# Kernel tuning notes

Measured on AMD Instinct MI355X. Metric: run time of the kernel, lower is better.

Reference implementation:

```python
import jax, jax.numpy as jnp
import numpy as np

KH = KW = 3
K = KH * KW
GROUPS = 8


def conv_same(x, w, b=None):
    out = jax.lax.conv_general_dilated(x, w, (1, 1), 'SAME',
                                       dimension_numbers=('NHWC', 'HWIO', 'NHWC'))
    if b is not None:
        out = out + b
    return out


def feature_selection(x, w_att, w_sel):
    pooled = x.mean(axis=(1, 2), keepdims=True)            # [B,1,1,C]
    attn = jax.nn.sigmoid(conv_same(pooled, w_att))        # 1x1 conv, sigmoid
    return conv_same(x * (attn + 1.0), w_sel)              # [B,H,W,F]


def deform_sample(x, sy, sx):
    # x: [H,W,G,Cg]; sy,sx: [H,W,G,K] fractional sample coords (zero outside)
    H, W, G, _ = x.shape
    y0 = jnp.floor(sy)
    x0 = jnp.floor(sx)
    wy1 = sy - y0
    wx1 = sx - x0
    gi = jnp.arange(G)[None, None, :, None]

    def gather(yi, xi):
        valid = (yi >= 0) & (yi <= H - 1) & (xi >= 0) & (xi <= W - 1)
        yc = jnp.clip(yi, 0, H - 1).astype(jnp.int32)
        xc = jnp.clip(xi, 0, W - 1).astype(jnp.int32)
        v = x[yc, xc, gi]                                   # [H,W,G,K,Cg]
        return v * valid[..., None]

    v00 = gather(y0, x0)
    v01 = gather(y0, x0 + 1)
    v10 = gather(y0 + 1, x0)
    v11 = gather(y0 + 1, x0 + 1)
    wy1 = wy1[..., None]
    wx1 = wx1[..., None]
    top = v00 * (1 - wx1) + v01 * wx1
    bot = v10 * (1 - wx1) + v11 * wx1
    return top * (1 - wy1) + bot * wy1                      # [H,W,G,K,Cg]


def dcnv2(x, align, w_om, b_om, w_dcn, b_dcn):
    # x: [B,H,W,C] input to deform-conv; align: [B,H,W,Ca] alignment feature
    B, H, W, C = x.shape
    G = GROUPS
    Cg = C // G
    om = conv_same(align, w_om, b_om)                       # [B,H,W,G*3*K]
    off = om[..., :G * 2 * K].reshape(B, H, W, G, K, 2)     # (dy, dx)
    mask = jax.nn.sigmoid(om[..., G * 2 * K:]).reshape(B, H, W, G, K)

    iy = jnp.arange(H, dtype=x.dtype)[:, None, None, None]
    ix = jnp.arange(W, dtype=x.dtype)[None, :, None, None]
    ky, kx = jnp.meshgrid(jnp.arange(KH) - (KH - 1) // 2,
                          jnp.arange(KW) - (KW - 1) // 2, indexing='ij')
    ky = ky.reshape(K).astype(x.dtype)
    kx = kx.reshape(K).astype(x.dtype)
    sy = iy + ky + off[..., 0]                              # [B,H,W,G,K]
    sx = ix + kx + off[..., 1]

    xg = x.reshape(B, H, W, G, Cg)
    sampled = jax.vmap(deform_sample)(xg, sy, sx)           # [B,H,W,G,K,Cg]
    sampled = sampled * mask[..., None]
    sampled = sampled.transpose(0, 1, 2, 4, 3, 5).reshape(B, H, W, K, C)
    wk = w_dcn.reshape(K, C, -1)                            # [K,C,F]
    return jnp.einsum('bhwkc,kcf->bhwf', sampled, wk) + b_dcn


def reference(coarse, fine, w_att, w_sel, w_off, w_om, b_om, w_dcn, b_dcn):
    B, H, W, _ = fine.shape
    coarse_up = jax.image.resize(coarse, (B, H, W, coarse.shape[-1]), 'bilinear')
    fine_cal = feature_selection(fine, w_att, w_sel)
    fc = jnp.concatenate([fine_cal, coarse_up * 2.0], axis=-1)
    align = conv_same(fc, w_off)                            # 1x1, no bias
    aligned = jax.nn.relu(dcnv2(coarse_up, align, w_om, b_om, w_dcn, b_dcn))
    return aligned + fine_cal


def setup_inputs() -> dict:
    key = jax.random.key(0)
    ks = jax.random.split(key, 8)
    B, H, W = 4, 64, 64
    Cc, Cf, F = 256, 256, 256
    s = lambda fan: (2.0 / fan) ** 0.5
    return {
        'coarse': jax.random.normal(ks[0], (B, H // 2, W // 2, Cc), jnp.float32),
        'fine': jax.random.normal(ks[1], (B, H, W, Cf), jnp.float32),
        'w_att': jax.random.normal(ks[2], (1, 1, Cf, Cf), jnp.float32) * s(Cf),
        'w_sel': jax.random.normal(ks[3], (1, 1, Cf, F), jnp.float32) * s(Cf),
        'w_off': jax.random.normal(ks[4], (1, 1, F + Cc, 2 * F), jnp.float32) * s(F + Cc),
        'w_om': jax.random.normal(ks[5], (3, 3, 2 * F, GROUPS * 3 * K), jnp.float32) * 0.01,
        'b_om': jnp.zeros((GROUPS * 3 * K,), jnp.float32),
        'w_dcn': jax.random.normal(ks[6], (3, 3, Cc, F), jnp.float32) * s(9 * Cc),
        'b_dcn': jnp.zeros((F,), jnp.float32),
    }
```

## Files before the change

kernel.cpp:

```cpp
#include <hip/hip_runtime.h>
#include <hip/hip_bf16.h>
#include <cstddef>

constexpr int HWP = 64 * 64;
constexpr int CCH = 256;
constexpr int OMC = 216;
constexpr int KDC = 2304;

typedef __attribute__((ext_vector_type(8))) short bf16x8;
typedef __attribute__((ext_vector_type(4))) float f32x4;

__device__ inline unsigned short f2bf(float x) {
  __hip_bfloat16 h = __float2bfloat16(x);
  return *reinterpret_cast<unsigned short*>(&h);
}
__device__ inline float bf2f(unsigned short u) {
  unsigned int v = ((unsigned int)u) << 16;
  return __uint_as_float(v);
}
__device__ inline void bfpair(unsigned int u, float& a, float& b) {
  a = __uint_as_float(u << 16);
  b = __uint_as_float(u & 0xffff0000u);
}

__global__ __launch_bounds__(256) void prep_weights(
    const float* __restrict__ w_off, const float* __restrict__ w_om,
    const float* __restrict__ w_sel, const float* __restrict__ w_dcn,
    unsigned short* __restrict__ w_offT, unsigned short* __restrict__ w_omT,
    unsigned short* __restrict__ w_selT, unsigned short* __restrict__ w_dcnT) {
  int i = blockIdx.x * 256 + threadIdx.x;
  if (i < 512 * 512) {
    int n = i >> 9, k = i & 511;
    w_offT[i] = f2bf(w_off[k * 512 + n]);
  }
  if (i < 9 * 256 * 512) {
    int c = i & 511;
    int r = i >> 9;
    int tap = r >> 8;
    int n = r & 255;
    w_omT[i] = f2bf(n < OMC ? w_om[((size_t)tap * 512 + c) * OMC + n] : 0.f);
  }
  if (i < 256 * 256) {
    int n = i >> 8, k = i & 255;
    w_selT[i] = f2bf(w_sel[k * 256 + n]);
  }
  if (i < 9 * 256 * 256) {
    int tap = i >> 16, f = (i >> 8) & 255, c = i & 255;
    w_dcnT[i] = f2bf(w_dcn[((size_t)tap * 256 + c) * 256 + f]);
  }
}

__global__ __launch_bounds__(256) void pool_partial(
    const float* __restrict__ fine, float* __restrict__ partial) {
  int r = blockIdx.x;
  int b = blockIdx.y;
  int t = threadIdx.x;
  const float* src = fine + ((size_t)b * 4096 + r * 64) * 256 + t;
  float s = 0.f;
#pragma unroll 8
  for (int p = 0; p < 64; ++p) s += src[(size_t)p * 256];
  partial[((size_t)b * 64 + r) * 256 + t] = s;
}

__global__ __launch_bounds__(256) void pool_finish(
    const float* __restrict__ partial, const float* __restrict__ w_att,
    float* __restrict__ scale) {
  __shared__ float pl[256];
  int b = blockIdx.x;
  int t = threadIdx.x;
  const float* pp = partial + (size_t)b * 64 * 256 + t;
  float s = 0.f;
#pragma unroll 8
  for (int r = 0; r < 64; ++r) s += pp[(size_t)r * 256];
  pl[t] = s * (1.0f / 4096.0f);
  __syncthreads();
  float acc = 0.f;
  for (int ci = 0; ci < 256; ++ci) acc += pl[ci] * w_att[ci * 256 + t];
  scale[b * 256 + t] = 1.0f + 1.0f / (1.0f + expf(-acc));
}

__global__ __launch_bounds__(256) void upsample_kernel(
    const float* __restrict__ coarse, unsigned short* __restrict__ upbf,
    unsigned short* __restrict__ alignA) {
  int m = blockIdx.x;
  int c = threadIdx.x;
  int b = m >> 12, h = (m >> 6) & 63, w = m & 63;
  float cy = fminf(fmaxf(h * 0.5f - 0.25f, 0.f), 31.f);
  float cx = fminf(fmaxf(w * 0.5f - 0.25f, 0.f), 31.f);
  int y0 = (int)cy, x0 = (int)cx;
  float fy = cy - y0, fx = cx - x0;
  int y1 = min(y0 + 1, 31), x1 = min(x0 + 1, 31);
  const float* base = coarse + (size_t)b * 32 * 32 * CCH;
  float v00 = base[(y0 * 32 + x0) * CCH + c];
  float v01 = base[(y0 * 32 + x1) * CCH + c];
  float v10 = base[(y1 * 32 + x0) * CCH + c];
  float v11 = base[(y1 * 32 + x1) * CCH + c];
  float top = v00 + (v01 - v00) * fx;
  float bot = v10 + (v11 - v10) * fx;
  float v = top + (bot - top) * fy;
  upbf[(size_t)m * CCH + c] = f2bf(v);
  alignA[(size_t)m * 512 + 256 + c] = f2bf(2.f * v);
}

__global__ __launch_bounds__(256) void gemm_finecal_mfma(
    const float* __restrict__ fine, const float* __restrict__ scale,
    const unsigned short* __restrict__ w_selT,
    float* __restrict__ finecal, unsigned short* __restrict__ alignA) {
  __shared__ unsigned short As[128][72];
  __shared__ unsigned short Bs[64][72];
  __shared__ float sc[256];
  int n0 = blockIdx.x * 64;
  int m0 = blockIdx.y * 128;
  int t = threadIdx.x;
  int wid = t >> 6, lane = t & 63;
  int lrow = lane & 15, lq = lane >> 4;
  int bb = m0 >> 12;
  sc[t] = scale[bb * 256 + t];
  f32x4 acc[2][4];
#pragma unroll
  for (int i = 0; i < 2; ++i)
#pragma unroll
    for (int j = 0; j < 4; ++j) acc[i][j] = (f32x4){0.f, 0.f, 0.f, 0.f};
  for (int k0 = 0; k0 < 256; k0 += 64) {
    __syncthreads();
    for (int u = t; u < 128 * 8; u += 256) {
      int row = u >> 3, ck = u & 7;
      const float* fp = &fine[(size_t)(m0 + row) * 256 + k0 + ck * 8];
      float4 f0 = *(const float4*)fp;
      float4 f1 = *(const float4*)(fp + 4);
      int kb = k0 + ck * 8;
      ushort4 u0 = make_ushort4(f2bf(f0.x * sc[kb]), f2bf(f0.y * sc[kb + 1]),
                                f2bf(f0.z * sc[kb + 2]), f2bf(f0.w * sc[kb + 3]));
      ushort4 u1 = make_ushort4(f2bf(f1.x * sc[kb + 4]), f2bf(f1.y * sc[kb + 5]),
                                f2bf(f1.z * sc[kb + 6]), f2bf(f1.w * sc[kb + 7]));
      *(ushort4*)&As[row][ck * 8] = u0;
      *(ushort4*)&As[row][ck * 8 + 4] = u1;
    }
    for (int u = t; u < 64 * 8; u += 256) {
      int row = u >> 3, ck = u & 7;
      *(uint4*)&Bs[row][ck * 8] = *(const uint4*)&w_selT[(size_t)(n0 + row) * 256 + k0 + ck * 8];
    }
    __syncthreads();
#pragma unroll
    for (int kk = 0; kk < 2; ++kk) {
      bf16x8 a[2], b[4];
#pragma unroll
      for (int mt = 0; mt < 2; ++mt)
        a[mt] = *(const bf16x8*)&As[wid * 32 + mt * 16 + lrow][kk * 32 + lq * 8];
#pragma unroll
      for (int nt = 0; nt < 4; ++nt)
        b[nt] = *(const bf16x8*)&Bs[nt * 16 + lrow][kk * 32 + lq * 8];
#pragma unroll
      for (int mt = 0; mt < 2; ++mt)
#pragma unroll
        for (int nt = 0; nt < 4; ++nt)
          acc[mt][nt] = __builtin_amdgcn_mfma_f32_16x16x32_bf16(
              a[mt], b[nt], acc[mt][nt], 0, 0, 0);
    }
  }
#pragma unroll
  for (int mt = 0; mt < 2; ++mt)
#pragma unroll
    for (int nt = 0; nt < 4; ++nt)
#pragma unroll
      for (int r = 0; r < 4; ++r) {
        int m = m0 + wid * 32 + mt * 16 + lq * 4 + r;
        int n = n0 + nt * 16 + lrow;
        finecal[(size_t)m * 256 + n] = acc[mt][nt][r];
        alignA[(size_t)m * 512 + n] = f2bf(acc[mt][nt][r]);
      }
}

__global__ __launch_bounds__(256) void gemm_align_mfma(
    const unsigned short* __restrict__ alignA,
    const unsigned short* __restrict__ w_offT,
    unsigned short* __restrict__ alignBf) {
  __shared__ unsigned short As[128][72];
  __shared__ unsigned short Bs[64][72];
  int n0 = blockIdx.x * 64;
  int m0 = blockIdx.y * 128;
  int t = threadIdx.x;
  int wid = t >> 6, lane = t & 63;
  int lrow = lane & 15, lq = lane >> 4;
  f32x4 acc[2][4];
#pragma unroll
  for (int i = 0; i < 2; ++i)
#pragma unroll
    for (int j = 0; j < 4; ++j) acc[i][j] = (f32x4){0.f, 0.f, 0.f, 0.f};
  for (int k0 = 0; k0 < 512; k0 += 64) {
    __syncthreads();
    for (int u = t; u < 128 * 8; u += 256) {
      int row = u >> 3, ck = u & 7;
      *(uint4*)&As[row][ck * 8] =
          *(const uint4*)&alignA[(size_t)(m0 + row) * 512 + k0 + ck * 8];
    }
    for (int u = t; u < 64 * 8; u += 256) {
      int row = u >> 3, ck = u & 7;
      *(uint4*)&Bs[row][ck * 8] =
          *(const uint4*)&w_offT[(size_t)(n0 + row) * 512 + k0 + ck * 8];
    }
    __syncthreads();
#pragma unroll
    for (int kk = 0; kk < 2; ++kk) {
      bf16x8 a[2], b[4];
#pragma unroll
      for (int mt = 0; mt < 2; ++mt)
        a[mt] = *(const bf16x8*)&As[wid * 32 + mt * 16 + lrow][kk * 32 + lq * 8];
#pragma unroll
      for (int nt = 0; nt < 4; ++nt)
        b[nt] = *(const bf16x8*)&Bs[nt * 16 + lrow][kk * 32 + lq * 8];
#pragma unroll
      for (int mt = 0; mt < 2; ++mt)
#pragma unroll
        for (int nt = 0; nt < 4; ++nt)
          acc[mt][nt] = __builtin_amdgcn_mfma_f32_16x16x32_bf16(
              a[mt], b[nt], acc[mt][nt], 0, 0, 0);
    }
  }
#pragma unroll
  for (int mt = 0; mt < 2; ++mt)
#pragma unroll
    for (int nt = 0; nt < 4; ++nt)
#pragma unroll
      for (int r = 0; r < 4; ++r) {
        int m = m0 + wid * 32 + mt * 16 + lq * 4 + r;
        int n = n0 + nt * 16 + lrow;
        alignBf[(size_t)m * 512 + n] = f2bf(acc[mt][nt][r]);
      }
}

__global__ __launch_bounds__(256) void om_conv_mfma(
    const unsigned short* __restrict__ alignBf,
    const unsigned short* __restrict__ w_omT,
    const float* __restrict__ b_om,
    float* __restrict__ om) {
  __shared__ unsigned short As[4][66][72];
  __shared__ unsigned short Bs[2][64][72];
  int nblk = blockIdx.x;
  int mblk = blockIdx.y;
  int b = mblk >> 5, hp = mblk & 31;
  int h0 = hp * 2;
  int n0 = nblk * 64;
  int t = threadIdx.x;
  int wid = t >> 6, lane = t & 63;
  int wy = wid >> 1, wx = wid & 1;
  int lrow = lane & 15, lq = lane >> 4;
  const size_t imgbase = (size_t)b * 4096;
  f32x4 acc[4][2];
#pragma unroll
  for (int i = 0; i < 4; ++i)
#pragma unroll
    for (int j = 0; j < 2; ++j) acc[i][j] = (f32x4){0.f, 0.f, 0.f, 0.f};

  int brow = t >> 3, bck = t & 7;
  uint4 pb[2];
  auto loadB = [&](int tap, int c0, uint4* p) {
#pragma unroll
    for (int i = 0; i < 2; ++i)
      p[i] = *(const uint4*)&w_omT[((size_t)tap * 256 + n0 + brow + i * 32) * 512 +
                                   c0 * 64 + bck * 8];
  };
  auto storeB = [&](int buf, const uint4* p) {
#pragma unroll
    for (int i = 0; i < 2; ++i)
      *(uint4*)&Bs[buf][brow + i * 32][bck * 8] = p[i];
  };
  auto stageA = [&](int c0) {
    for (int u = t; u < 4 * 66 * 8; u += 256) {
      int dy = u / 528;
      int r = u - dy * 528;
      int px = r >> 3, ck = r & 7;
      int w = px - 1;
      int y = h0 - 1 + dy;
      uint4 v = make_uint4(0u, 0u, 0u, 0u);
      if (w >= 0 && w < 64 && y >= 0 && y < 64)
        v = *(const uint4*)&alignBf[(imgbase + y * 64 + w) * 512 + c0 * 64 + ck * 8];
      *(uint4*)&As[dy][px][ck * 8] = v;
    }
  };

  loadB(0, 0, pb);
  storeB(0, pb);
  stageA(0);
  __syncthreads();
  int buf = 0;
  for (int c0 = 0; c0 < 8; ++c0) {
    for (int tap = 0; tap < 9; ++tap) {
      int ntap = tap + 1, nc0 = c0;
      bool has_next = true;
      if (ntap == 9) { ntap = 0; nc0 = c0 + 1; has_next = (nc0 < 8); }
      if (has_next) loadB(ntap, nc0, pb);
      int dyt = tap / 3, dxt = tap - dyt * 3;
#pragma unroll
      for (int kk = 0; kk < 2; ++kk) {
        bf16x8 a[4], bb[2];
#pragma unroll
        for (int mt = 0; mt < 4; ++mt)
          a[mt] = *(const bf16x8*)&As[wy + dyt][mt * 16 + lrow + dxt][kk * 32 + lq * 8];
#pragma unroll
        for (int nt = 0; nt < 2; ++nt)
          bb[nt] = *(const bf16x8*)&Bs[buf][wx * 32 + nt * 16 + lrow][kk * 32 + lq * 8];
#pragma unroll
        for (int mt = 0; mt < 4; ++mt)
#pragma unroll
          for (int nt = 0; nt < 2; ++nt)
            acc[mt][nt] = __builtin_amdgcn_mfma_f32_16x16x32_bf16(
                a[mt], bb[nt], acc[mt][nt], 0, 0, 0);
      }
      if (has_next) {
        storeB(buf ^ 1, pb);
        __syncthreads();
        buf ^= 1;
        if (tap == 8) {
          stageA(nc0);
          __syncthreads();
        }
      }
    }
  }
#pragma unroll
  for (int nt = 0; nt < 2; ++nt) {
    int n = n0 + wx * 32 + nt * 16 + lrow;
    if (n < OMC) {
      float bias = b_om[n];
#pragma unroll
      for (int mt = 0; mt < 4; ++mt) {
#pragma unroll
        for (int r = 0; r < 4; ++r) {
          size_t m = imgbase + (size_t)(h0 + wy) * 64 + mt * 16 + lq * 4 + r;
          om[m * OMC + n] = acc[mt][nt][r] + bias;
        }
      }
    }
  }
}

__global__ __launch_bounds__(256) void dcn_sample(
    const float* __restrict__ om, const unsigned short* __restrict__ upbf,
    unsigned short* __restrict__ S, int bh0) {
  __shared__ int offsA[256][4];
  __shared__ float wtsA[256][4];
  int blk = blockIdx.x;
  int bh = bh0 + (blk >> 1);
  int half = blk & 1;
  int b = bh >> 6, h = bh & 63;
  int p0 = half * 32;
  int m0g = bh * 64 + p0;
  int mloc0 = (bh - bh0) * 64 + p0;
  int t = threadIdx.x;
  const unsigned short* upb = upbf + (size_t)b * HWP * CCH;
  int lane = t & 63;
  int ph = t >> 6;
  int c = lane * 4;
  int g = lane >> 3;
  for (int tap = 0; tap < 9; ++tap) {
    int ky = tap / 3, kx = tap - ky * 3;
    __syncthreads();
    {
      int p = t >> 3, gg = t & 7;
      const float* omr = om + (size_t)(m0g + p) * OMC;
      float dy = omr[gg * 18 + tap * 2];
      float dx = omr[gg * 18 + tap * 2 + 1];
      float mk = 1.0f / (1.0f + expf(-omr[144 + gg * 9 + tap]));
      float sy = (float)(h + ky - 1) + dy;
      float sx = (float)(p0 + p + kx - 1) + dx;
      float y0f = floorf(sy), x0f = floorf(sx);
      float fy = sy - y0f, fx = sx - x0f;
      int y0 = (int)y0f, x0 = (int)x0f;
      int y1 = y0 + 1, x1 = x0 + 1;
      float vy0 = (y0 >= 0 && y0 <= 63) ? 1.f : 0.f;
      float vy1 = (y1 >= 0 && y1 <= 63) ? 1.f : 0.f;
      float vx0 = (x0 >= 0 && x0 <= 63) ? 1.f : 0.f;
      float vx1 = (x1 >= 0 && x1 <= 63) ? 1.f : 0.f;
      int yc0 = min(max(y0, 0), 63), yc1 = min(max(y1, 0), 63);
      int xc0 = min(max(x0, 0), 63), xc1 = min(max(x1, 0), 63);
      offsA[t][0] = (yc0 * 64 + xc0) * 256;
      offsA[t][1] = (yc0 * 64 + xc1) * 256;
      offsA[t][2] = (yc1 * 64 + xc0) * 256;
      offsA[t][3] = (yc1 * 64 + xc1) * 256;
      wtsA[t][0] = (1.f - fy) * (1.f - fx) * vy0 * vx0 * mk;
      wtsA[t][1] = (1.f - fy) * fx * vy0 * vx1 * mk;
      wtsA[t][2] = fy * (1.f - fx) * vy1 * vx0 * mk;
      wtsA[t][3] = fy * fx * vy1 * vx1 * mk;
    }
    __syncthreads();
#pragma unroll
    for (int pp = 0; pp < 8; ++pp) {
      int p = ph * 8 + pp;
      int idx = (p << 3) | g;
      int4 o = *(const int4*)&offsA[idx][0];
      float4 wv = *(const float4*)&wtsA[idx][0];
      uint2 u00 = *(const uint2*)&upb[o.x + c];
      uint2 u01 = *(const uint2*)&upb[o.y + c];
      uint2 u10 = *(const uint2*)&upb[o.z + c];
      uint2 u11 = *(const uint2*)&upb[o.w + c];
      float a0, a1, a2, a3, b0, b1, b2, b3, c0, c1, c2, c3, d0, d1, d2, d3;
      bfpair(u00.x, a0, a1); bfpair(u00.y, a2, a3);
      bfpair(u01.x, b0, b1); bfpair(u01.y, b2, b3);
      bfpair(u10.x, c0, c1); bfpair(u10.y, c2, c3);
      bfpair(u11.x, d0, d1); bfpair(u11.y, d2, d3);
      float v0 = wv.x * a0 + wv.y * b0 + wv.z * c0 + wv.w * d0;
      float v1 = wv.x * a1 + wv.y * b1 + wv.z * c1 + wv.w * d1;
      float v2 = wv.x * a2 + wv.y * b2 + wv.z * c2 + wv.w * d2;
      float v3 = wv.x * a3 + wv.y * b3 + wv.z * c3 + wv.w * d3;
      uint2 outv;
      outv.x = (unsigned int)f2bf(v0) | ((unsigned int)f2bf(v1) << 16);
      outv.y = (unsigned int)f2bf(v2) | ((unsigned int)f2bf(v3) << 16);
      *(uint2*)&S[(size_t)(mloc0 + p) * KDC + tap * 256 + c] = outv;
    }
  }
}

__global__ __launch_bounds__(256) void dcn_gemm(
    const unsigned short* __restrict__ S,
    const unsigned short* __restrict__ w_dcnT,
    const float* __restrict__ b_dcn,
    const float* __restrict__ finecal,
    float* __restrict__ outp, int m_base, int kiters) {
  __shared__ unsigned short As[2][64][72];
  __shared__ unsigned short Bs[2][128][72];
  int n0 = blockIdx.x * 128;
  int mloc0 = blockIdx.y * 64;
  int m0 = m_base + mloc0;
  int t = threadIdx.x;
  int wid = t >> 6, lane = t & 63;
  int wy = wid >> 1, wx = wid & 1;
  int lrow = lane & 15, lq = lane >> 4;
  f32x4 acc[2][4];
#pragma unroll
  for (int i = 0; i < 2; ++i)
#pragma unroll
    for (int j = 0; j < 4; ++j) acc[i][j] = (f32x4){0.f, 0.f, 0.f, 0.f};

  int arow = t >> 3, ack = t & 7;
  uint4 pa[2], pb[4];
  auto loadA = [&](int k0, uint4* p) {
#pragma unroll
    for (int i = 0; i < 2; ++i)
      p[i] = *(const uint4*)&S[(size_t)(mloc0 + arow + i * 32) * KDC + k0 + ack * 8];
  };
  auto loadB = [&](int k0, uint4* p) {
    int tap = k0 >> 8, c0 = k0 & 255;
#pragma unroll
    for (int i = 0; i < 4; ++i)
      p[i] = *(const uint4*)&w_dcnT[((size_t)tap * 256 + n0 + arow + i * 32) * 256 + c0 + ack * 8];
  };
  auto storeTiles = [&](int buf, const uint4* a, const uint4* b) {
#pragma unroll
    for (int i = 0; i < 2; ++i)
      *(uint4*)&As[buf][arow + i * 32][ack * 8] = a[i];
#pragma unroll
    for (int i = 0; i < 4; ++i)
      *(uint4*)&Bs[buf][arow + i * 32][ack * 8] = b[i];
  };

  loadA(0, pa);
  loadB(0, pb);
  storeTiles(0, pa, pb);
  __syncthreads();
  int buf = 0;
  for (int kb = 0; kb < kiters; ++kb) {
    bool has_next = (kb + 1) < kiters;
    if (has_next) {
      loadA((kb + 1) * 64, pa);
      loadB((kb + 1) * 64, pb);
    }
#pragma unroll
    for (int kk = 0; kk < 2; ++kk) {
      bf16x8 a[2], b[4];
#pragma unroll
      for (int mt = 0; mt < 2; ++mt)
        a[mt] = *(const bf16x8*)&As[buf][wy * 32 + mt * 16 + lrow][kk * 32 + lq * 8];
#pragma unroll
      for (int nt = 0; nt < 4; ++nt)
        b[nt] = *(const bf16x8*)&Bs[buf][wx * 64 + nt * 16 + lrow][kk * 32 + lq * 8];
#pragma unroll
      for (int mt = 0; mt < 2; ++mt)
#pragma unroll
        for (int nt = 0; nt < 4; ++nt)
          acc[mt][nt] = __builtin_amdgcn_mfma_f32_16x16x32_bf16(
              a[mt], b[nt], acc[mt][nt], 0, 0, 0);
    }
    if (has_next) {
      storeTiles(buf ^ 1, pa, pb);
      __syncthreads();
      buf ^= 1;
    }
  }
#pragma unroll
  for (int mt = 0; mt < 2; ++mt)
#pragma unroll
    for (int nt = 0; nt < 4; ++nt) {
      int f = n0 + wx * 64 + nt * 16 + lrow;
      float bias = b_dcn[f];
#pragma unroll
      for (int r = 0; r < 4; ++r) {
        int m = m0 + wy * 32 + mt * 16 + lq * 4 + r;
        float v = fmaxf(acc[mt][nt][r] + bias, 0.f);
        float fc = __builtin_nontemporal_load(&finecal[(size_t)m * 256 + f]);
        __builtin_nontemporal_store(v + fc, &outp[(size_t)m * 256 + f]);
      }
    }
}

extern "C" void kernel_launch(void* const* d_in, const int* in_sizes, int n_in,
                              void* d_out, int out_size, void* d_ws, size_t ws_size,
                              hipStream_t stream) {
  const float* coarse = (const float*)d_in[0];
  const float* fine   = (const float*)d_in[1];
  const float* w_att  = (const float*)d_in[2];
  const float* w_sel  = (const float*)d_in[3];
  const float* w_off  = (const float*)d_in[4];
  const float* w_om   = (const float*)d_in[5];
  const float* b_om   = (const float*)d_in[6];
  const float* w_dcn  = (const float*)d_in[7];
  const float* b_dcn  = (const float*)d_in[8];
  float* outp = (float*)d_out;

  char* base = (char*)d_ws;
  size_t o = 0;
  float* scale            = (float*)(base + o);          o += 4096;
  float* finecal          = (float*)(base + o);          o += 16777216;
  float* omb              = (float*)(base + o);          o += 14155776;
  unsigned short* upbf    = (unsigned short*)(base + o); o += 8388608;
  unsigned short* w_offT  = (unsigned short*)(base + o); o += 524288;
  unsigned short* w_omT   = (unsigned short*)(base + o); o += 2359296;
  unsigned short* w_selT  = (unsigned short*)(base + o); o += 131072;
  unsigned short* w_dcnT  = (unsigned short*)(base + o); o += 1179648;
  unsigned short* Sbuf    = (unsigned short*)(base + o);
  size_t fixed = o;
  unsigned short* alignA  = Sbuf;
  unsigned short* alignBf = (unsigned short*)((char*)Sbuf + 16777216);
  float* partial = omb;

  bool fullS = (ws_size >= fixed + 75497472);

  prep_weights<<<dim3(4608), dim3(256), 0, stream>>>(
      w_off, w_om, w_sel, w_dcn, w_offT, w_omT, w_selT, w_dcnT);
  pool_partial<<<dim3(64, 4), dim3(256), 0, stream>>>(fine, partial);
  pool_finish<<<dim3(4), dim3(256), 0, stream>>>(partial, w_att, scale);
  upsample_kernel<<<dim3(16384), dim3(256), 0, stream>>>(coarse, upbf, alignA);
  gemm_finecal_mfma<<<dim3(4, 128), dim3(256), 0, stream>>>(
      fine, scale, w_selT, finecal, alignA);
  gemm_align_mfma<<<dim3(8, 128), dim3(256), 0, stream>>>(alignA, w_offT, alignBf);
  om_conv_mfma<<<dim3(4, 128), dim3(256), 0, stream>>>(alignBf, w_omT, b_om, omb);

  if (fullS) {
    dcn_sample<<<dim3(512), dim3(256), 0, stream>>>(omb, upbf, Sbuf, 0);
    dcn_gemm<<<dim3(2, 256), dim3(256), 0, stream>>>(
        Sbuf, w_dcnT, b_dcn, finecal, outp, 0, KDC / 64);
  } else {
    for (int ch = 0; ch < 2; ++ch) {
      dcn_sample<<<dim3(256), dim3(256), 0, stream>>>(omb, upbf, Sbuf, ch * 128);
      dcn_gemm<<<dim3(2, 128), dim3(256), 0, stream>>>(
          Sbuf, w_dcnT, b_dcn, finecal, outp, ch * 8192, KDC / 64);
    }
  }
}
```

Before: 426.3 us.

## Register-prefetch next K tile in GEMMs and simplify om_conv B staging

Both 1x1 GEMM kernels now load the next K-slice of A and B into registers while the MFMAs run on the current shared tile, then write it to shared memory between barriers. The goal is to hide global load latency behind compute. The om_conv kernel drops its register prefetch of weights and instead writes the next tap's weights directly into the alternate shared buffer before computing, moving the A restaging outside the tap loop. This adds register pressure in the GEMMs, and om_conv now does one extra redundant B stage at the end.

```diff
diff --git a/kernel.cpp b/kernel.cpp
--- a/kernel.cpp
+++ b/kernel.cpp
@@ -121,26 +121,49 @@
   for (int i = 0; i < 2; ++i)
 #pragma unroll
     for (int j = 0; j < 4; ++j) acc[i][j] = (f32x4){0.f, 0.f, 0.f, 0.f};
-  for (int k0 = 0; k0 < 256; k0 += 64) {
-    __syncthreads();
-    for (int u = t; u < 128 * 8; u += 256) {
-      int row = u >> 3, ck = u & 7;
-      const float* fp = &fine[(size_t)(m0 + row) * 256 + k0 + ck * 8];
-      float4 f0 = *(const float4*)fp;
-      float4 f1 = *(const float4*)(fp + 4);
-      int kb = k0 + ck * 8;
-      ushort4 u0 = make_ushort4(f2bf(f0.x * sc[kb]), f2bf(f0.y * sc[kb + 1]),
-                                f2bf(f0.z * sc[kb + 2]), f2bf(f0.w * sc[kb + 3]));
-      ushort4 u1 = make_ushort4(f2bf(f1.x * sc[kb + 4]), f2bf(f1.y * sc[kb + 5]),
-                                f2bf(f1.z * sc[kb + 6]), f2bf(f1.w * sc[kb + 7]));
-      *(ushort4*)&As[row][ck * 8] = u0;
-      *(ushort4*)&As[row][ck * 8 + 4] = u1;
-    }
-    for (int u = t; u < 64 * 8; u += 256) {
-      int row = u >> 3, ck = u & 7;
-      *(uint4*)&Bs[row][ck * 8] = *(const uint4*)&w_selT[(size_t)(n0 + row) * 256 + k0 + ck * 8];
-    }
-    __syncthreads();
+
+  int arow = t >> 3, ack = t & 7;
+  float4 paf[4][2];
+  uint4 pb[2];
+  auto loadA = [&](int k0) {
+#pragma unroll
+    for (int i = 0; i < 4; ++i) {
+      const float* fp = &fine[(size_t)(m0 + arow + i * 32) * 256 + k0 + ack * 8];
+      paf[i][0] = *(const float4*)fp;
+      paf[i][1] = *(const float4*)(fp + 4);
+    }
+  };
+  auto loadB = [&](int k0) {
+#pragma unroll
+    for (int i = 0; i < 2; ++i)
+      pb[i] = *(const uint4*)&w_selT[(size_t)(n0 + arow + i * 32) * 256 + k0 + ack * 8];
+  };
+  auto storeT = [&](int k0) {
+    int kb = k0 + ack * 8;
+    float s0 = sc[kb], s1 = sc[kb + 1], s2 = sc[kb + 2], s3 = sc[kb + 3];
+    float s4 = sc[kb + 4], s5 = sc[kb + 5], s6 = sc[kb + 6], s7 = sc[kb + 7];
+#pragma unroll
+    for (int i = 0; i < 4; ++i) {
+      ushort4 u0 = make_ushort4(f2bf(paf[i][0].x * s0), f2bf(paf[i][0].y * s1),
+                                f2bf(paf[i][0].z * s2), f2bf(paf[i][0].w * s3));
+      ushort4 u1 = make_ushort4(f2bf(paf[i][1].x * s4), f2bf(paf[i][1].y * s5),
+                                f2bf(paf[i][1].z * s6), f2bf(paf[i][1].w * s7));
+      *(ushort4*)&As[arow + i * 32][ack * 8] = u0;
+      *(ushort4*)&As[arow + i * 32][ack * 8 + 4] = u1;
+    }
+#pragma unroll
+    for (int i = 0; i < 2; ++i)
+      *(uint4*)&Bs[arow + i * 32][ack * 8] = pb[i];
+  };
+
+  loadA(0);
+  loadB(0);
+  __syncthreads();
+  storeT(0);
+  __syncthreads();
+  for (int kb = 0; kb < 4; ++kb) {
+    bool has_next = (kb + 1) < 4;
+    if (has_next) { loadA((kb + 1) * 64); loadB((kb + 1) * 64); }
 #pragma unroll
     for (int kk = 0; kk < 2; ++kk) {
       bf16x8 a[2], b[4];
@@ -156,6 +179,11 @@
         for (int nt = 0; nt < 4; ++nt)
           acc[mt][nt] = __builtin_amdgcn_mfma_f32_16x16x32_bf16(
               a[mt], b[nt], acc[mt][nt], 0, 0, 0);
+    }
+    if (has_next) {
+      __syncthreads();
+      storeT((kb + 1) * 64);
+      __syncthreads();
     }
   }
 #pragma unroll
@@ -187,19 +215,35 @@
   for (int i = 0; i < 2; ++i)
 #pragma unroll
     for (int j = 0; j < 4; ++j) acc[i][j] = (f32x4){0.f, 0.f, 0.f, 0.f};
-  for (int k0 = 0; k0 < 512; k0 += 64) {
-    __syncthreads();
-    for (int u = t; u < 128 * 8; u += 256) {
-      int row = u >> 3, ck = u & 7;
-      *(uint4*)&As[row][ck * 8] =
-          *(const uint4*)&alignA[(size_t)(m0 + row) * 512 + k0 + ck * 8];
-    }
-    for (int u = t; u < 64 * 8; u += 256) {
-      int row = u >> 3, ck = u & 7;
-      *(uint4*)&Bs[row][ck * 8] =
-          *(const uint4*)&w_offT[(size_t)(n0 + row) * 512 + k0 + ck * 8];
-    }
-    __syncthreads();
+
+  int arow = t >> 3, ack = t & 7;
+  uint4 pa[4], pb[2];
+  auto loadA = [&](int k0) {
+#pragma unroll
+    for (int i = 0; i < 4; ++i)
+      pa[i] = *(const uint4*)&alignA[(size_t)(m0 + arow + i * 32) * 512 + k0 + ack * 8];
+  };
+  auto loadB = [&](int k0) {
+#pragma unroll
+    for (int i = 0; i < 2; ++i)
+      pb[i] = *(const uint4*)&w_offT[(size_t)(n0 + arow + i * 32) * 512 + k0 + ack * 8];
+  };
+  auto storeT = [&]() {
+#pragma unroll
+    for (int i = 0; i < 4; ++i)
+      *(uint4*)&As[arow + i * 32][ack * 8] = pa[i];
+#pragma unroll
+    for (int i = 0; i < 2; ++i)
+      *(uint4*)&Bs[arow + i * 32][ack * 8] = pb[i];
+  };
+
+  loadA(0);
+  loadB(0);
+  storeT();
+  __syncthreads();
+  for (int kb = 0; kb < 8; ++kb) {
+    bool has_next = (kb + 1) < 8;
+    if (has_next) { loadA((kb + 1) * 64); loadB((kb + 1) * 64); }
 #pragma unroll
     for (int kk = 0; kk < 2; ++kk) {
       bf16x8 a[2], b[4];
@@ -215,6 +259,11 @@
         for (int nt = 0; nt < 4; ++nt)
           acc[mt][nt] = __builtin_amdgcn_mfma_f32_16x16x32_bf16(
               a[mt], b[nt], acc[mt][nt], 0, 0, 0);
+    }
+    if (has_next) {
+      __syncthreads();
+      storeT();
+      __syncthreads();
     }
   }
 #pragma unroll
@@ -252,18 +301,12 @@
 #pragma unroll
     for (int j = 0; j < 2; ++j) acc[i][j] = (f32x4){0.f, 0.f, 0.f, 0.f};
 
-  int brow = t >> 3, bck = t & 7;
-  uint4 pb[2];
-  auto loadB = [&](int tap, int c0, uint4* p) {
-#pragma unroll
-    for (int i = 0; i < 2; ++i)
-      p[i] = *(const uint4*)&w_omT[((size_t)tap * 256 + n0 + brow + i * 32) * 512 +
-                                   c0 * 64 + bck * 8];
-  };
-  auto storeB = [&](int buf, const uint4* p) {
-#pragma unroll
-    for (int i = 0; i < 2; ++i)
-      *(uint4*)&Bs[buf][brow + i * 32][bck * 8] = p[i];
+  auto stageB = [&](int buf, int tap, int c0) {
+    for (int u = t; u < 64 * 8; u += 256) {
+      int n = u >> 3, ck = u & 7;
+      *(uint4*)&Bs[buf][n][ck * 8] =
+          *(const uint4*)&w_omT[((size_t)tap * 256 + n0 + n) * 512 + c0 * 64 + ck * 8];
+    }
   };
   auto stageA = [&](int c0) {
     for (int u = t; u < 4 * 66 * 8; u += 256) {
@@ -279,17 +322,15 @@
     }
   };
 
-  loadB(0, 0, pb);
-  storeB(0, pb);
+  stageB(0, 0, 0);
   stageA(0);
   __syncthreads();
   int buf = 0;
   for (int c0 = 0; c0 < 8; ++c0) {
     for (int tap = 0; tap < 9; ++tap) {
       int ntap = tap + 1, nc0 = c0;
-      bool has_next = true;
-      if (ntap == 9) { ntap = 0; nc0 = c0 + 1; has_next = (nc0 < 8); }
-      if (has_next) loadB(ntap, nc0, pb);
+      if (ntap == 9) { ntap = 0; nc0 = (c0 + 1) & 7; }
+      stageB(buf ^ 1, ntap, nc0);
       int dyt = tap / 3, dxt = tap - dyt * 3;
 #pragma unroll
       for (int kk = 0; kk < 2; ++kk) {
@@ -307,15 +348,12 @@
             acc[mt][nt] = __builtin_amdgcn_mfma_f32_16x16x32_bf16(
                 a[mt], bb[nt], acc[mt][nt], 0, 0, 0);
       }
-      if (has_next) {
-        storeB(buf ^ 1, pb);
-        __syncthreads();
-        buf ^= 1;
-        if (tap == 8) {
-          stageA(nc0);
-          __syncthreads();
-        }
-      }
+      __syncthreads();
+      buf ^= 1;
+    }
+    if (c0 < 7) {
+      stageA(c0 + 1);
+      __syncthreads();
     }
   }
 #pragma unroll
```

Result: slower. 451.5 us (+5.9%).
